# Performance work log

Hardware: AMD Instinct MI355X
Metric: run time of the kernel (lower is better)

## Reference

```python
import jax, jax.numpy as jnp
import numpy as np

N_NODES = 100000


def _gcn_conv(h, src, dst, norm, b, num_nodes):
    # h: [N, D] already linearly transformed; aggregate norm-weighted messages at dst
    msgs = norm[:, None] * h[src]                      # [E+N, D] gather
    out = jax.ops.segment_sum(msgs, dst, num_segments=num_nodes)  # scatter-add
    return out + b


def _norm_and_loops(edge_index, num_nodes):
    # add self-loops and compute symmetric degree normalization (GCNConv default)
    loop = jnp.arange(num_nodes, dtype=edge_index.dtype)
    src = jnp.concatenate([edge_index[0], loop])
    dst = jnp.concatenate([edge_index[1], loop])
    deg = jax.ops.segment_sum(jnp.ones_like(dst, dtype=jnp.float32), dst,
                              num_segments=num_nodes)
    dinv = jnp.where(deg > 0, jax.lax.rsqrt(jnp.maximum(deg, 1.0)), 0.0)
    norm = dinv[src] * dinv[dst]
    return src, dst, norm


def setup_inputs() -> dict:
    key = jax.random.key(0)
    k1, k2, k3, k4 = jax.random.split(key, 4)
    x = jax.random.normal(k1, (N_NODES, 512), dtype=jnp.float32)
    edge_index = jax.random.randint(k2, (2, 3200000), 0, N_NODES, dtype=jnp.int64)
    W1 = jax.random.normal(k3, (512, 16), dtype=jnp.float32) * (1.0 / np.sqrt(512))
    b1 = jnp.zeros((16,), dtype=jnp.float32)
    W2 = jax.random.normal(k4, (16, 7), dtype=jnp.float32) * (1.0 / np.sqrt(16))
    b2 = jnp.zeros((7,), dtype=jnp.float32)
    return {"x": x, "edge_index": edge_index, "W1": W1, "b1": b1, "W2": W2, "b2": b2}


def reference(x, edge_index, W1, b1, W2, b2):
    n = x.shape[0]
    src, dst, norm = _norm_and_loops(edge_index, n)
    h = _gcn_conv(x @ W1, src, dst, norm, b1, n)   # layer 1
    h = jax.nn.relu(h)                              # dropout off in eval mode
    h = _gcn_conv(h @ W2, src, dst, norm, b2, n)   # layer 2
    return jax.nn.log_softmax(h, axis=1)
```

## Files before the change

kernel.cpp:

```cpp
#include <hip/hip_runtime.h>
#include <hip/hip_bf16.h>


#define N_NODES 100000
#define NPAD    100352
#define D_IN    512
#define H1DIM   16
#define C_OUT   7
#define C_PAD   8

#define NB      196
#define NBUCK   512
#define BCAP    8192
#define TILE_A  8192


__global__ __launch_bounds__(256) void k_zinit(int* __restrict__ bcount) {
    int i = blockIdx.x * 256 + threadIdx.x;
    if (i < NBUCK) bcount[i] = 0;
}

__global__ __launch_bounds__(256) void k_bhist(const int* __restrict__ dst, int E,
                                               int* __restrict__ bcount) {
    __shared__ int h[NBUCK];
    for (int i = threadIdx.x; i < NBUCK; i += 256) h[i] = 0;
    __syncthreads();
    int stride = gridDim.x * 256;
    for (int e = blockIdx.x * 256 + threadIdx.x; e < E; e += stride)
        atomicAdd(&h[(unsigned)dst[e] / NB], 1);
    __syncthreads();
    for (int i = threadIdx.x; i < NBUCK; i += 256) {
        int v = h[i];
        if (v) atomicAdd(&bcount[i], v);
    }
}

__global__ void k_bscan(const int* __restrict__ bcount, int* __restrict__ bbase,
                        int* __restrict__ cursor) {
    __shared__ int sm[NBUCK];
    int t = threadIdx.x;
    int c = bcount[t];
    sm[t] = c;
    __syncthreads();
    for (int off = 1; off < NBUCK; off <<= 1) {
        int v = (t >= off) ? sm[t - off] : 0;
        __syncthreads();
        sm[t] += v;
        __syncthreads();
    }
    int excl = sm[t] - c;
    bbase[t] = excl;
    cursor[t] = excl;
    if (t == NBUCK - 1) bbase[NBUCK] = sm[t];
}

__global__ __launch_bounds__(512) void k_passA(const int* __restrict__ src,
                                               const int* __restrict__ dst, int E,
                                               int* __restrict__ cursor,
                                               unsigned* __restrict__ packed) {
    __shared__ int hist[NBUCK];
    __shared__ int wp[NBUCK];
    int tile0 = blockIdx.x * TILE_A;
    for (int i = threadIdx.x; i < NBUCK; i += 512) hist[i] = 0;
    __syncthreads();
    unsigned pay[16];
    unsigned short bk[16];
#pragma unroll
    for (int r = 0; r < 16; ++r) {
        int e = tile0 + r * 512 + threadIdx.x;
        if (e < E) {
            unsigned d = (unsigned)dst[e];
            unsigned s = (unsigned)src[e];
            unsigned b = d / NB;
            pay[r] = ((d - b * NB) << 17) | s;
            bk[r] = (unsigned short)b;
            atomicAdd(&hist[b], 1);
        } else {
            bk[r] = 0xffffu;
        }
    }
    __syncthreads();
    if (threadIdx.x < NBUCK) {
        int c = hist[threadIdx.x];
        wp[threadIdx.x] = (c > 0) ? atomicAdd(&cursor[threadIdx.x], c) : 0;
    }
    __syncthreads();
#pragma unroll
    for (int r = 0; r < 16; ++r) {
        if (bk[r] != 0xffffu) {
            int pos = atomicAdd(&wp[bk[r]], 1);
            packed[pos] = pay[r];
        }
    }
}

__global__ __launch_bounds__(256) void k_passB(const unsigned* __restrict__ packed,
                                               const int* __restrict__ bbase,
                                               int* __restrict__ sorted_src,
                                               int* __restrict__ offs,
                                               int* __restrict__ cnt_out,
                                               float* __restrict__ dinv) {
    __shared__ unsigned ent[BCAP];
    __shared__ int sorted[BCAP];
    __shared__ int hist[NB + 1];
    __shared__ int scan[NB + 1];
    __shared__ int wp[NB];
    int b = blockIdx.x;
    int base = bbase[b];
    int cnt = bbase[b + 1] - base;
    if (cnt > BCAP) cnt = BCAP;
    for (int i = threadIdx.x; i < cnt; i += 256) ent[i] = packed[base + i];
    for (int i = threadIdx.x; i <= NB; i += 256) hist[i] = 0;
    __syncthreads();
    for (int i = threadIdx.x; i < cnt; i += 256) atomicAdd(&hist[ent[i] >> 17], 1);
    __syncthreads();
    if (threadIdx.x <= NB)
        scan[threadIdx.x] = (threadIdx.x == 0) ? 0 : hist[threadIdx.x - 1];
    __syncthreads();
    for (int off = 1; off < 256; off <<= 1) {
        int v = 0;
        if (threadIdx.x <= NB && threadIdx.x >= off) v = scan[threadIdx.x - off];
        __syncthreads();
        if (threadIdx.x <= NB) scan[threadIdx.x] += v;
        __syncthreads();
    }
    int node0 = b * NB;
    if (threadIdx.x < NB) {
        int node = node0 + threadIdx.x;
        if (node < N_NODES) {
            int h = hist[threadIdx.x];
            cnt_out[node] = h;
            offs[node] = base + scan[threadIdx.x];
            dinv[node] = rsqrtf(1.0f + (float)h);
        }
        wp[threadIdx.x] = scan[threadIdx.x];
    }
    __syncthreads();
    for (int i = threadIdx.x; i < cnt; i += 256) {
        unsigned p = ent[i];
        int dl = (int)(p >> 17);
        int pos = atomicAdd(&wp[dl], 1);
        sorted[pos] = (int)(p & 0x1FFFFu);
    }
    __syncthreads();
    for (int i = threadIdx.x; i < cnt; i += 256) sorted_src[base + i] = sorted[i];
}


__global__ __launch_bounds__(128) void k_gemm1(const float* __restrict__ x,
                                               const float* __restrict__ W1,
                                               const float* __restrict__ b1,
                                               const float* __restrict__ dinv,
                                               float* __restrict__ h1,
                                               float* __restrict__ out1) {
    int row = blockIdx.x * 128 + threadIdx.x;
    if (row >= N_NODES) return;
    const float4* x4 = (const float4*)(x + (size_t)row * D_IN);
    const float4* W14 = (const float4*)W1;
    float acc[16];
#pragma unroll
    for (int k = 0; k < 16; ++k) acc[k] = 0.0f;

#pragma unroll 4
    for (int d4 = 0; d4 < D_IN / 4; ++d4) {
        float4 xv = x4[d4];
#pragma unroll
        for (int r = 0; r < 4; ++r) {
            int d = d4 * 4 + r;
            float xs = (r == 0) ? xv.x : (r == 1) ? xv.y : (r == 2) ? xv.z : xv.w;
#pragma unroll
            for (int q = 0; q < 4; ++q) {
                float4 w = W14[d * 4 + q];
                acc[q * 4 + 0] = fmaf(xs, w.x, acc[q * 4 + 0]);
                acc[q * 4 + 1] = fmaf(xs, w.y, acc[q * 4 + 1]);
                acc[q * 4 + 2] = fmaf(xs, w.z, acc[q * 4 + 2]);
                acc[q * 4 + 3] = fmaf(xs, w.w, acc[q * 4 + 3]);
            }
        }
    }

    float di = dinv[row];
    float di2 = di * di;
    float4* h14 = (float4*)(h1 + (size_t)row * H1DIM);
    float4* o14 = (float4*)(out1 + (size_t)row * H1DIM);
    const float4* b14 = (const float4*)b1;
#pragma unroll
    for (int q = 0; q < 4; ++q) {
        float4 a;
        a.x = acc[q * 4 + 0]; a.y = acc[q * 4 + 1];
        a.z = acc[q * 4 + 2]; a.w = acc[q * 4 + 3];
        h14[q] = a;
        float4 bq = b14[q];
        float4 o;
        o.x = fmaf(di2, a.x, bq.x);
        o.y = fmaf(di2, a.y, bq.y);
        o.z = fmaf(di2, a.z, bq.z);
        o.w = fmaf(di2, a.w, bq.w);
        o14[q] = o;
    }
}

__global__ __launch_bounds__(256) void k_msg1(const int* __restrict__ offs,
                                              const int* __restrict__ count,
                                              const int* __restrict__ sorted_src,
                                              const float* __restrict__ dinv,
                                              const float* __restrict__ h1,
                                              float* __restrict__ out1) {
    int node = blockIdx.x * 4 + (threadIdx.x >> 6);
    if (node >= N_NODES) return;
    int lane = threadIdx.x & 63;
    int s = lane >> 4;
    int k = lane & 15;
    int off = offs[node];
    int cnt = count[node];
    float dvi = dinv[node];
    float acc = 0.0f;
    for (int c = s; c < cnt; c += 4) {
        int sv = sorted_src[off + c];
        float w = dinv[sv] * dvi;
        acc = fmaf(w, h1[(size_t)sv * H1DIM + k], acc);
    }
    acc += __shfl_xor(acc, 16);
    acc += __shfl_xor(acc, 32);
    if (s == 0) out1[(size_t)node * H1DIM + k] += acc;
}

__global__ __launch_bounds__(256) void k_gemm2(const float* __restrict__ out1,
                                               const float* __restrict__ W2,
                                               const float* __restrict__ b2,
                                               const float* __restrict__ dinv,
                                               float* __restrict__ h2,
                                               float* __restrict__ out2) {
    int i = blockIdx.x * 256 + threadIdx.x;
    if (i >= N_NODES) return;
    const float4* o14 = (const float4*)(out1 + (size_t)i * H1DIM);
    float v[16];
#pragma unroll
    for (int q = 0; q < 4; ++q) {
        float4 a = o14[q];
        v[q * 4 + 0] = fmaxf(a.x, 0.0f);
        v[q * 4 + 1] = fmaxf(a.y, 0.0f);
        v[q * 4 + 2] = fmaxf(a.z, 0.0f);
        v[q * 4 + 3] = fmaxf(a.w, 0.0f);
    }
    float h[7];
#pragma unroll
    for (int j = 0; j < 7; ++j) h[j] = 0.0f;
#pragma unroll
    for (int k = 0; k < 16; ++k) {
#pragma unroll
        for (int j = 0; j < 7; ++j) h[j] = fmaf(v[k], W2[k * 7 + j], h[j]);
    }
    float di = dinv[i];
    float di2 = di * di;
    float* h2r = h2 + (size_t)i * C_PAD;
    float* o2r = out2 + (size_t)i * C_PAD;
#pragma unroll
    for (int j = 0; j < 7; ++j) {
        h2r[j] = h[j];
        o2r[j] = fmaf(di2, h[j], b2[j]);
    }
    h2r[7] = 0.0f;
    o2r[7] = 0.0f;
}

__global__ __launch_bounds__(256) void k_msg2(const int* __restrict__ offs,
                                              const int* __restrict__ count,
                                              const int* __restrict__ sorted_src,
                                              const float* __restrict__ dinv,
                                              const float* __restrict__ h2,
                                              float* __restrict__ out2) {
    int node = blockIdx.x * 4 + (threadIdx.x >> 6);
    if (node >= N_NODES) return;
    int lane = threadIdx.x & 63;
    int s = lane >> 3;
    int j = lane & 7;
    int off = offs[node];
    int cnt = count[node];
    float dvi = dinv[node];
    float acc = 0.0f;
    for (int c = s; c < cnt; c += 8) {
        int sv = sorted_src[off + c];
        float w = dinv[sv] * dvi;
        acc = fmaf(w, h2[(size_t)sv * C_PAD + j], acc);
    }
    acc += __shfl_xor(acc, 8);
    acc += __shfl_xor(acc, 16);
    acc += __shfl_xor(acc, 32);
    if (s == 0) out2[(size_t)node * C_PAD + j] += acc;
}

__global__ __launch_bounds__(256) void k_logsm(const float* __restrict__ out2,
                                               float* __restrict__ out) {
    int i = blockIdx.x * 256 + threadIdx.x;
    if (i >= N_NODES) return;
    const float* r = out2 + (size_t)i * C_PAD;
    float v[7];
#pragma unroll
    for (int j = 0; j < 7; ++j) v[j] = r[j];
    float m = v[0];
#pragma unroll
    for (int j = 1; j < 7; ++j) m = fmaxf(m, v[j]);
    float ssum = 0.0f;
#pragma unroll
    for (int j = 0; j < 7; ++j) ssum += expf(v[j] - m);
    float l = logf(ssum);
    float* o = out + (size_t)i * C_OUT;
#pragma unroll
    for (int j = 0; j < 7; ++j) o[j] = v[j] - m - l;
}


extern "C" void kernel_launch(void* const* d_in, const int* in_sizes, int n_in,
                              void* d_out, int out_size, void* d_ws, size_t ws_size,
                              hipStream_t stream) {
    const float* x  = (const float*)d_in[0];
    const int*   ei = (const int*)d_in[1];
    const float* W1 = (const float*)d_in[2];
    const float* b1 = (const float*)d_in[3];
    const float* W2 = (const float*)d_in[4];
    const float* b2 = (const float*)d_in[5];
    float* out = (float*)d_out;

    const int E = in_sizes[1] / 2;
    const int* src = ei;
    const int* dst = ei + E;

    char* w = (char*)d_ws;
    size_t off = 0;
    auto alloc = [&](size_t bytes) -> void* {
        off = (off + 255) & ~(size_t)255;
        void* p = w + off;
        off += bytes;
        return p;
    };
    int*   bcount     = (int*)alloc(NBUCK * 4);
    int*   bbase      = (int*)alloc((NBUCK + 1) * 4);
    int*   cursor     = (int*)alloc(NBUCK * 4);
    int*   count      = (int*)alloc(NPAD * 4);
    int*   offs       = (int*)alloc(NPAD * 4);
    float* dinv       = (float*)alloc(NPAD * 4);
    int*   sorted_src = (int*)alloc((size_t)E * 4);
    float* h1   = (float*)alloc((size_t)N_NODES * H1DIM * 4);
    float* out1 = (float*)alloc((size_t)N_NODES * H1DIM * 4);
    float* h2   = (float*)alloc((size_t)N_NODES * C_PAD * 4);
    float* out2 = (float*)alloc((size_t)N_NODES * C_PAD * 4);
    (void)ws_size;
    unsigned* packed = (unsigned*)h1;

    const int gN4 = (N_NODES + 3) / 4;
    const int gN256 = (N_NODES + 255) / 256;
    const int gA = (E + TILE_A - 1) / TILE_A;

    k_zinit<<<(NBUCK + 255) / 256, 256, 0, stream>>>(bcount);
    k_bhist<<<512, 256, 0, stream>>>(dst, E, bcount);
    k_bscan<<<1, NBUCK, 0, stream>>>(bcount, bbase, cursor);
    k_passA<<<gA, 512, 0, stream>>>(src, dst, E, cursor, packed);
    k_passB<<<NBUCK, 256, 0, stream>>>(packed, bbase, sorted_src, offs, count, dinv);

    k_gemm1<<<(N_NODES + 127) / 128, 128, 0, stream>>>(x, W1, b1, dinv, h1, out1);
    k_msg1<<<gN4, 256, 0, stream>>>(offs, count, sorted_src, dinv, h1, out1);
    k_gemm2<<<gN256, 256, 0, stream>>>(out1, W2, b2, dinv, h2, out2);
    k_msg2<<<gN4, 256, 0, stream>>>(offs, count, sorted_src, dinv, h2, out2);
    k_logsm<<<gN256, 256, 0, stream>>>(out2, out);
}
```

Measured before the change: 540.4 us.

## Drop bucket histogram pass, fuse GCN layers with gemm2 and log-softmax

Replaces the global histogram and scan with fixed-capacity buckets (BCAP slots per bucket), so the bucket-count pass over dst is gone. gemm1 now stages W1 in LDS with a rotated layout and splits each row across 4 lanes. The layer-1 aggregation is fused with bias, ReLU and the 16x7 gemm2, and the layer-2 aggregation is fused with log-softmax. This drops several launches and the intermediate out1/out2 round trips. The cost is that buckets holding more than BCAP edges are silently truncated, and the packed and sorted buffers take more workspace.

```diff
diff --git a/kernel.cpp b/kernel.cpp
--- a/kernel.cpp
+++ b/kernel.cpp
@@ -6,52 +6,16 @@
 #define NPAD    100352
 #define D_IN    512
 #define H1DIM   16
-#define C_OUT   7
 #define C_PAD   8
-
 #define NB      196
 #define NBUCK   512
 #define BCAP    8192
 #define TILE_A  8192
 
 
-__global__ __launch_bounds__(256) void k_zinit(int* __restrict__ bcount) {
+__global__ __launch_bounds__(256) void k_initcur(int* __restrict__ cursor) {
     int i = blockIdx.x * 256 + threadIdx.x;
-    if (i < NBUCK) bcount[i] = 0;
-}
-
-__global__ __launch_bounds__(256) void k_bhist(const int* __restrict__ dst, int E,
-                                               int* __restrict__ bcount) {
-    __shared__ int h[NBUCK];
-    for (int i = threadIdx.x; i < NBUCK; i += 256) h[i] = 0;
-    __syncthreads();
-    int stride = gridDim.x * 256;
-    for (int e = blockIdx.x * 256 + threadIdx.x; e < E; e += stride)
-        atomicAdd(&h[(unsigned)dst[e] / NB], 1);
-    __syncthreads();
-    for (int i = threadIdx.x; i < NBUCK; i += 256) {
-        int v = h[i];
-        if (v) atomicAdd(&bcount[i], v);
-    }
-}
-
-__global__ void k_bscan(const int* __restrict__ bcount, int* __restrict__ bbase,
-                        int* __restrict__ cursor) {
-    __shared__ int sm[NBUCK];
-    int t = threadIdx.x;
-    int c = bcount[t];
-    sm[t] = c;
-    __syncthreads();
-    for (int off = 1; off < NBUCK; off <<= 1) {
-        int v = (t >= off) ? sm[t - off] : 0;
-        __syncthreads();
-        sm[t] += v;
-        __syncthreads();
-    }
-    int excl = sm[t] - c;
-    bbase[t] = excl;
-    cursor[t] = excl;
-    if (t == NBUCK - 1) bbase[NBUCK] = sm[t];
+    if (i < NBUCK) cursor[i] = i * BCAP;
 }
 
 __global__ __launch_bounds__(512) void k_passA(const int* __restrict__ src,
@@ -80,22 +44,23 @@
         }
     }
     __syncthreads();
-    if (threadIdx.x < NBUCK) {
+    {
         int c = hist[threadIdx.x];
-        wp[threadIdx.x] = (c > 0) ? atomicAdd(&cursor[threadIdx.x], c) : 0;
+        wp[threadIdx.x] = c ? atomicAdd(&cursor[threadIdx.x], c) : 0;
     }
     __syncthreads();
 #pragma unroll
     for (int r = 0; r < 16; ++r) {
         if (bk[r] != 0xffffu) {
             int pos = atomicAdd(&wp[bk[r]], 1);
-            packed[pos] = pay[r];
+            int lim = ((int)bk[r] + 1) * BCAP;
+            if (pos < lim) packed[pos] = pay[r];
         }
     }
 }
 
 __global__ __launch_bounds__(256) void k_passB(const unsigned* __restrict__ packed,
-                                               const int* __restrict__ bbase,
+                                               const int* __restrict__ cursor,
                                                int* __restrict__ sorted_src,
                                                int* __restrict__ offs,
                                                int* __restrict__ cnt_out,
@@ -106,8 +71,8 @@
     __shared__ int scan[NB + 1];
     __shared__ int wp[NB];
     int b = blockIdx.x;
-    int base = bbase[b];
-    int cnt = bbase[b + 1] - base;
+    int base = b * BCAP;
+    int cnt = cursor[b] - base;
     if (cnt > BCAP) cnt = BCAP;
     for (int i = threadIdx.x; i < cnt; i += 256) ent[i] = packed[base + i];
     for (int i = threadIdx.x; i <= NB; i += 256) hist[i] = 0;
@@ -138,8 +103,7 @@
     __syncthreads();
     for (int i = threadIdx.x; i < cnt; i += 256) {
         unsigned p = ent[i];
-        int dl = (int)(p >> 17);
-        int pos = atomicAdd(&wp[dl], 1);
+        int pos = atomicAdd(&wp[p >> 17], 1);
         sorted[pos] = (int)(p & 0x1FFFFu);
     }
     __syncthreads();
@@ -147,167 +111,129 @@
 }
 
 
-__global__ __launch_bounds__(128) void k_gemm1(const float* __restrict__ x,
-                                               const float* __restrict__ W1,
-                                               const float* __restrict__ b1,
-                                               const float* __restrict__ dinv,
-                                               float* __restrict__ h1,
-                                               float* __restrict__ out1) {
-    int row = blockIdx.x * 128 + threadIdx.x;
+__global__ __launch_bounds__(256) void k_gemm1(const float* __restrict__ x,
+                                               const float4* __restrict__ W14,
+                                               float* __restrict__ h1) {
+    __shared__ float4 Wl[2048];
+    for (int g = threadIdx.x; g < 2048; g += 256) {
+        int d = g >> 2, q = g & 3;
+        Wl[d * 4 + ((q + (d >> 2)) & 3)] = W14[g];
+    }
+    int row = blockIdx.x * 64 + (threadIdx.x >> 2);
+    int sub = threadIdx.x & 3;
+    __syncthreads();
     if (row >= N_NODES) return;
-    const float4* x4 = (const float4*)(x + (size_t)row * D_IN);
-    const float4* W14 = (const float4*)W1;
+    const float4* xr = (const float4*)(x + (size_t)row * D_IN);
     float acc[16];
 #pragma unroll
     for (int k = 0; k < 16; ++k) acc[k] = 0.0f;
 
-#pragma unroll 4
-    for (int d4 = 0; d4 < D_IN / 4; ++d4) {
-        float4 xv = x4[d4];
+#pragma unroll 2
+    for (int i = 0; i < 32; ++i) {
+        int d4 = sub + i * 4;
+        float4 xv = xr[d4];
+        int rot = d4 & 3;
 #pragma unroll
         for (int r = 0; r < 4; ++r) {
             int d = d4 * 4 + r;
             float xs = (r == 0) ? xv.x : (r == 1) ? xv.y : (r == 2) ? xv.z : xv.w;
 #pragma unroll
             for (int q = 0; q < 4; ++q) {
-                float4 w = W14[d * 4 + q];
-                acc[q * 4 + 0] = fmaf(xs, w.x, acc[q * 4 + 0]);
-                acc[q * 4 + 1] = fmaf(xs, w.y, acc[q * 4 + 1]);
-                acc[q * 4 + 2] = fmaf(xs, w.z, acc[q * 4 + 2]);
-                acc[q * 4 + 3] = fmaf(xs, w.w, acc[q * 4 + 3]);
+                float4 wv = Wl[d * 4 + ((q + rot) & 3)];
+                acc[q * 4 + 0] = fmaf(xs, wv.x, acc[q * 4 + 0]);
+                acc[q * 4 + 1] = fmaf(xs, wv.y, acc[q * 4 + 1]);
+                acc[q * 4 + 2] = fmaf(xs, wv.z, acc[q * 4 + 2]);
+                acc[q * 4 + 3] = fmaf(xs, wv.w, acc[q * 4 + 3]);
             }
         }
     }
-
-    float di = dinv[row];
-    float di2 = di * di;
-    float4* h14 = (float4*)(h1 + (size_t)row * H1DIM);
-    float4* o14 = (float4*)(out1 + (size_t)row * H1DIM);
-    const float4* b14 = (const float4*)b1;
-#pragma unroll
-    for (int q = 0; q < 4; ++q) {
-        float4 a;
-        a.x = acc[q * 4 + 0]; a.y = acc[q * 4 + 1];
-        a.z = acc[q * 4 + 2]; a.w = acc[q * 4 + 3];
-        h14[q] = a;
-        float4 bq = b14[q];
-        float4 o;
-        o.x = fmaf(di2, a.x, bq.x);
-        o.y = fmaf(di2, a.y, bq.y);
-        o.z = fmaf(di2, a.z, bq.z);
-        o.w = fmaf(di2, a.w, bq.w);
-        o14[q] = o;
-    }
-}
-
-__global__ __launch_bounds__(256) void k_msg1(const int* __restrict__ offs,
-                                              const int* __restrict__ count,
-                                              const int* __restrict__ sorted_src,
-                                              const float* __restrict__ dinv,
-                                              const float* __restrict__ h1,
-                                              float* __restrict__ out1) {
+#pragma unroll
+    for (int k = 0; k < 16; ++k) {
+        acc[k] += __shfl_xor(acc[k], 1);
+        acc[k] += __shfl_xor(acc[k], 2);
+    }
+    float4 o;
+    if (sub == 0)      o = make_float4(acc[0],  acc[1],  acc[2],  acc[3]);
+    else if (sub == 1) o = make_float4(acc[4],  acc[5],  acc[6],  acc[7]);
+    else if (sub == 2) o = make_float4(acc[8],  acc[9],  acc[10], acc[11]);
+    else               o = make_float4(acc[12], acc[13], acc[14], acc[15]);
+    ((float4*)(h1 + (size_t)row * H1DIM))[sub] = o;
+}
+
+__global__ __launch_bounds__(256) void k_msg1g2(const int* __restrict__ offs,
+                                                const int* __restrict__ cnt_,
+                                                const int* __restrict__ ssrc,
+                                                const float* __restrict__ dinv,
+                                                const float* __restrict__ h1,
+                                                const float* __restrict__ b1,
+                                                const float* __restrict__ W2,
+                                                float* __restrict__ h2) {
     int node = blockIdx.x * 4 + (threadIdx.x >> 6);
     if (node >= N_NODES) return;
     int lane = threadIdx.x & 63;
     int s = lane >> 4;
     int k = lane & 15;
     int off = offs[node];
-    int cnt = count[node];
-    float dvi = dinv[node];
+    int cnt = cnt_[node];
     float acc = 0.0f;
     for (int c = s; c < cnt; c += 4) {
-        int sv = sorted_src[off + c];
-        float w = dinv[sv] * dvi;
-        acc = fmaf(w, h1[(size_t)sv * H1DIM + k], acc);
+        int sv = ssrc[off + c];
+        acc = fmaf(dinv[sv], h1[(size_t)sv * H1DIM + k], acc);
     }
     acc += __shfl_xor(acc, 16);
     acc += __shfl_xor(acc, 32);
-    if (s == 0) out1[(size_t)node * H1DIM + k] += acc;
-}
-
-__global__ __launch_bounds__(256) void k_gemm2(const float* __restrict__ out1,
-                                               const float* __restrict__ W2,
-                                               const float* __restrict__ b2,
-                                               const float* __restrict__ dinv,
-                                               float* __restrict__ h2,
-                                               float* __restrict__ out2) {
-    int i = blockIdx.x * 256 + threadIdx.x;
-    if (i >= N_NODES) return;
-    const float4* o14 = (const float4*)(out1 + (size_t)i * H1DIM);
-    float v[16];
-#pragma unroll
-    for (int q = 0; q < 4; ++q) {
-        float4 a = o14[q];
-        v[q * 4 + 0] = fmaxf(a.x, 0.0f);
-        v[q * 4 + 1] = fmaxf(a.y, 0.0f);
-        v[q * 4 + 2] = fmaxf(a.z, 0.0f);
-        v[q * 4 + 3] = fmaxf(a.w, 0.0f);
-    }
-    float h[7];
-#pragma unroll
-    for (int j = 0; j < 7; ++j) h[j] = 0.0f;
-#pragma unroll
-    for (int k = 0; k < 16; ++k) {
-#pragma unroll
-        for (int j = 0; j < 7; ++j) h[j] = fmaf(v[k], W2[k * 7 + j], h[j]);
-    }
-    float di = dinv[i];
-    float di2 = di * di;
-    float* h2r = h2 + (size_t)i * C_PAD;
-    float* o2r = out2 + (size_t)i * C_PAD;
-#pragma unroll
-    for (int j = 0; j < 7; ++j) {
-        h2r[j] = h[j];
-        o2r[j] = fmaf(di2, h[j], b2[j]);
-    }
-    h2r[7] = 0.0f;
-    o2r[7] = 0.0f;
-}
-
-__global__ __launch_bounds__(256) void k_msg2(const int* __restrict__ offs,
-                                              const int* __restrict__ count,
-                                              const int* __restrict__ sorted_src,
-                                              const float* __restrict__ dinv,
-                                              const float* __restrict__ h2,
-                                              float* __restrict__ out2) {
+    float di = dinv[node];
+    float v = fmaf(di, acc, fmaf(di * di, h1[(size_t)node * H1DIM + k], b1[k]));
+    v = fmaxf(v, 0.0f);
+    int j = lane & 7, kh = lane >> 3;
+    float t1 = __shfl(v, kh);
+    float t2 = __shfl(v, kh + 8);
+    float w1 = (j < 7) ? W2[kh * 7 + j] : 0.0f;
+    float w2 = (j < 7) ? W2[(kh + 8) * 7 + j] : 0.0f;
+    float p = t1 * w1 + t2 * w2;
+    p += __shfl_xor(p, 8);
+    p += __shfl_xor(p, 16);
+    p += __shfl_xor(p, 32);
+    if (lane < 8) h2[(size_t)node * C_PAD + j] = (j < 7) ? p : 0.0f;
+}
+
+__global__ __launch_bounds__(256) void k_msg2sm(const int* __restrict__ offs,
+                                                const int* __restrict__ cnt_,
+                                                const int* __restrict__ ssrc,
+                                                const float* __restrict__ dinv,
+                                                const float* __restrict__ h2,
+                                                const float* __restrict__ b2,
+                                                float* __restrict__ out) {
     int node = blockIdx.x * 4 + (threadIdx.x >> 6);
     if (node >= N_NODES) return;
     int lane = threadIdx.x & 63;
     int s = lane >> 3;
     int j = lane & 7;
     int off = offs[node];
-    int cnt = count[node];
-    float dvi = dinv[node];
+    int cnt = cnt_[node];
     float acc = 0.0f;
     for (int c = s; c < cnt; c += 8) {
-        int sv = sorted_src[off + c];
-        float w = dinv[sv] * dvi;
-        acc = fmaf(w, h2[(size_t)sv * C_PAD + j], acc);
+        int sv = ssrc[off + c];
+        acc = fmaf(dinv[sv], h2[(size_t)sv * C_PAD + j], acc);
     }
     acc += __shfl_xor(acc, 8);
     acc += __shfl_xor(acc, 16);
     acc += __shfl_xor(acc, 32);
-    if (s == 0) out2[(size_t)node * C_PAD + j] += acc;
-}
-
-__global__ __launch_bounds__(256) void k_logsm(const float* __restrict__ out2,
-                                               float* __restrict__ out) {
-    int i = blockIdx.x * 256 + threadIdx.x;
-    if (i >= N_NODES) return;
-    const float* r = out2 + (size_t)i * C_PAD;
-    float v[7];
-#pragma unroll
-    for (int j = 0; j < 7; ++j) v[j] = r[j];
-    float m = v[0];
-#pragma unroll
-    for (int j = 1; j < 7; ++j) m = fmaxf(m, v[j]);
-    float ssum = 0.0f;
-#pragma unroll
-    for (int j = 0; j < 7; ++j) ssum += expf(v[j] - m);
-    float l = logf(ssum);
-    float* o = out + (size_t)i * C_OUT;
-#pragma unroll
-    for (int j = 0; j < 7; ++j) o[j] = v[j] - m - l;
+    float di = dinv[node];
+    float v = (j < 7)
+        ? fmaf(di, acc, fmaf(di * di, h2[(size_t)node * C_PAD + j], b2[j]))
+        : -INFINITY;
+    float m = v;
+    m = fmaxf(m, __shfl_xor(m, 1));
+    m = fmaxf(m, __shfl_xor(m, 2));
+    m = fmaxf(m, __shfl_xor(m, 4));
+    float e = expf(v - m);
+    float ss = e;
+    ss += __shfl_xor(ss, 1);
+    ss += __shfl_xor(ss, 2);
+    ss += __shfl_xor(ss, 4);
+    float r = v - m - logf(ss);
+    if (s == 0 && j < 7) out[(size_t)node * 7 + j] = r;
 }
 
 
@@ -334,33 +260,24 @@
         off += bytes;
         return p;
     };
-    int*   bcount     = (int*)alloc(NBUCK * 4);
-    int*   bbase      = (int*)alloc((NBUCK + 1) * 4);
-    int*   cursor     = (int*)alloc(NBUCK * 4);
-    int*   count      = (int*)alloc(NPAD * 4);
-    int*   offs       = (int*)alloc(NPAD * 4);
-    float* dinv       = (float*)alloc(NPAD * 4);
-    int*   sorted_src = (int*)alloc((size_t)E * 4);
-    float* h1   = (float*)alloc((size_t)N_NODES * H1DIM * 4);
-    float* out1 = (float*)alloc((size_t)N_NODES * H1DIM * 4);
-    float* h2   = (float*)alloc((size_t)N_NODES * C_PAD * 4);
-    float* out2 = (float*)alloc((size_t)N_NODES * C_PAD * 4);
+    int*      cursor     = (int*)alloc(NBUCK * 4);
+    int*      count      = (int*)alloc(NPAD * 4);
+    int*      offs       = (int*)alloc(NPAD * 4);
+    float*    dinv       = (float*)alloc(NPAD * 4);
+    unsigned* packed     = (unsigned*)alloc((size_t)NBUCK * BCAP * 4);
+    int*      sorted_src = (int*)alloc((size_t)NBUCK * BCAP * 4);
+    float*    h1         = (float*)alloc((size_t)N_NODES * H1DIM * 4);
+    float*    h2         = (float*)alloc((size_t)N_NODES * C_PAD * 4);
     (void)ws_size;
-    unsigned* packed = (unsigned*)h1;
-
+
+    const int gA = (E + TILE_A - 1) / TILE_A;
     const int gN4 = (N_NODES + 3) / 4;
-    const int gN256 = (N_NODES + 255) / 256;
-    const int gA = (E + TILE_A - 1) / TILE_A;
-
-    k_zinit<<<(NBUCK + 255) / 256, 256, 0, stream>>>(bcount);
-    k_bhist<<<512, 256, 0, stream>>>(dst, E, bcount);
-    k_bscan<<<1, NBUCK, 0, stream>>>(bcount, bbase, cursor);
+
+    k_initcur<<<(NBUCK + 255) / 256, 256, 0, stream>>>(cursor);
     k_passA<<<gA, 512, 0, stream>>>(src, dst, E, cursor, packed);
-    k_passB<<<NBUCK, 256, 0, stream>>>(packed, bbase, sorted_src, offs, count, dinv);
-
-    k_gemm1<<<(N_NODES + 127) / 128, 128, 0, stream>>>(x, W1, b1, dinv, h1, out1);
-    k_msg1<<<gN4, 256, 0, stream>>>(offs, count, sorted_src, dinv, h1, out1);
-    k_gemm2<<<gN256, 256, 0, stream>>>(out1, W2, b2, dinv, h2, out2);
-    k_msg2<<<gN4, 256, 0, stream>>>(offs, count, sorted_src, dinv, h2, out2);
-    k_logsm<<<gN256, 256, 0, stream>>>(out2, out);
-}
+    k_passB<<<NBUCK, 256, 0, stream>>>(packed, cursor, sorted_src, offs, count, dinv);
+
+    k_gemm1<<<(N_NODES + 63) / 64, 256, 0, stream>>>(x, (const float4*)W1, h1);
+    k_msg1g2<<<gN4, 256, 0, stream>>>(offs, count, sorted_src, dinv, h1, b1, W2, h2);
+    k_msg2sm<<<gN4, 256, 0, stream>>>(offs, count, sorted_src, dinv, h2, b2, out);
+}
```

After: 496.4 us. -8.1%, faster.
